# Kernel optimization log

Hardware: AMD Instinct MI355X
Metric: run time of the kernel (lower is better)

Reference implementation:

```python
import jax, jax.numpy as jnp
import numpy as np

LAM = 0.001  # init kwarg lam; agg='mean'


def setup_inputs() -> dict:
    key = jax.random.key(0)
    k1, k2 = jax.random.split(key)
    B, C, N = 4, 2, 8192
    inputs = jax.random.normal(k1, (B, C, N), dtype=jnp.float32)
    coords = jax.random.normal(k2, (B, N, 3), dtype=jnp.float32)
    return {"inputs": inputs, "coords": coords}


def _pairwise_dist(c):
    # c: (B, N, 3) -> (B, N, N) Euclidean distances (cdist p=2)
    sq = jnp.sum(c * c, axis=-1)                      # (B, N)
    d2 = sq[:, :, None] + sq[:, None, :] - 2.0 * jnp.einsum('bnd,bmd->bnm', c, c)
    return jnp.sqrt(jnp.maximum(d2, 0.0))


def reference(inputs, coords):
    coords = coords[:, :, :3]
    d = _pairwise_dist(coords)                        # (B, N, N)
    w = jax.nn.softmax(inputs, axis=1)[:, 1, :]       # (B, N) foreground prob
    dpp = d * w[:, :, None] * w[:, None, :]
    return jnp.mean(dpp) * LAM
```

## Files before the change

### kernel.cpp

```cpp
#include <hip/hip_runtime.h>

#define NFULL 8192
#define BATCH 4
#define NPTS (NFULL * BATCH)
#define TT 256
#define NT (NFULL / TT)
#define JOBS_PER_B (NT * (NT + 1) / 2)
#define TOTAL_JOBS (BATCH * JOBS_PER_B)
#define IR 4
#define IR2 (IR / 2)
#define JW 64
#define LAMBDA 0.001

typedef float f32x2 __attribute__((ext_vector_type(2)));

#define WS_PTS_OFF   0
#define WS_W_OFF     (NPTS * 16)
#define WS_PART_OFF  (WS_W_OFF + NPTS * 4)

__global__ __launch_bounds__(256)
void KUNi_prep(const float* __restrict__ inputs,
               const float* __restrict__ coords,
               float4* __restrict__ pts,
               float* __restrict__ wts) {
    const int idx = blockIdx.x * 256 + threadIdx.x;
    const int b = idx >> 13;
    const int n = idx & (NFULL - 1);
    const float* cp = coords + (size_t)idx * 3;
    const float x = cp[0], y = cp[1], z = cp[2];
    const float sq = fmaf(x, x, fmaf(y, y, z * z));
    const float a0 = inputs[(size_t)b * 2 * NFULL + n];
    const float a1 = inputs[(size_t)b * 2 * NFULL + NFULL + n];
    const float w = 1.0f / (1.0f + __expf(a0 - a1));
    pts[idx] = make_float4(x, y, z, sq);
    wts[idx] = w;
}

__global__ void KUNi_finalize(const float* __restrict__ partials,
                              float* __restrict__ out) {
    const int tid = threadIdx.x;
    const int lane = tid & 63, wv = tid >> 6;
    double s = 0.0;
    for (int i = tid; i < TOTAL_JOBS; i += 256) s += (double)partials[i];
#pragma unroll
    for (int off = 32; off > 0; off >>= 1) s += __shfl_xor(s, off, 64);
    __shared__ double sd[4];
    if (lane == 0) sd[wv] = s;
    __syncthreads();
    if (tid == 0) {
        const double scale = LAMBDA / ((double)BATCH * (double)NFULL * (double)NFULL);
        out[0] = (float)((sd[0] + sd[1] + sd[2] + sd[3]) * scale);
    }
}

__device__ __forceinline__ int tri_off(int t) {
    return t * (2 * NT + 1 - t) / 2;
}

__global__ __launch_bounds__(256)
void KUNi_dpp_kernel(const float4* __restrict__ pts,
                     const float* __restrict__ wts,
                     float* __restrict__ partials) {
    __shared__ float sred[4];

    const int tid = threadIdx.x;
    const int lane = tid & 63;
    const int wv = tid >> 6;
    const int bid = blockIdx.x;
    const int b = bid / JOBS_PER_B;
    const int p = bid - b * JOBS_PER_B;

    const float q = (float)(2 * NT + 1);
    int ti = (int)floorf((q - sqrtf(fmaf(-8.0f, (float)p, q * q))) * 0.5f);
    if (p < tri_off(ti)) --ti;
    else if (p >= tri_off(ti + 1)) ++ti;
    const int tj = ti + (p - tri_off(ti));
    const int base = b * NFULL;

    f32x2 ix2[IR2], iy2[IR2], iz2[IR2], isq2[IR2], iw2[IR2], acc2[IR2];
    const int ibase = base + ti * TT + lane;
#pragma unroll
    for (int k = 0; k < IR2; ++k) {
        const float4 p0 = pts[ibase + (2 * k) * 64];
        const float4 p1 = pts[ibase + (2 * k + 1) * 64];
        ix2[k]  = (f32x2){-2.0f * p0.x, -2.0f * p1.x};
        iy2[k]  = (f32x2){-2.0f * p0.y, -2.0f * p1.y};
        iz2[k]  = (f32x2){-2.0f * p0.z, -2.0f * p1.z};
        isq2[k] = (f32x2){p0.w, p1.w};
        iw2[k]  = (f32x2){wts[ibase + (2 * k) * 64],
                          wts[ibase + (2 * k + 1) * 64]};
        acc2[k] = (f32x2){0.0f, 0.0f};
    }

    const float4* __restrict__ pj = pts + base + tj * TT;
    const float* __restrict__ pw = wts + base + tj * TT;
    const int j0 = wv * JW;
#pragma unroll 4
    for (int jj = j0; jj < j0 + JW; ++jj) {
        const int ju = __builtin_amdgcn_readfirstlane(jj);
        const float4 jv = pj[ju];
        const float jw = pw[ju];
#pragma unroll
        for (int k = 0; k < IR2; ++k) {
            f32x2 t = isq2[k] + jv.w;
            t = __builtin_elementwise_fma(ix2[k], (f32x2){jv.x, jv.x}, t);
            t = __builtin_elementwise_fma(iy2[k], (f32x2){jv.y, jv.y}, t);
            t = __builtin_elementwise_fma(iz2[k], (f32x2){jv.z, jv.z}, t);
            t = __builtin_elementwise_max(t, (f32x2){0.0f, 0.0f});
            f32x2 s;
            s.x = __builtin_amdgcn_sqrtf(t.x);
            s.y = __builtin_amdgcn_sqrtf(t.y);
            acc2[k] = __builtin_elementwise_fma(s, (f32x2){jw, jw}, acc2[k]);
        }
    }

    f32x2 vv = iw2[0] * acc2[0];
#pragma unroll
    for (int k = 1; k < IR2; ++k)
        vv = __builtin_elementwise_fma(iw2[k], acc2[k], vv);
    float v = vv.x + vv.y;
    if (ti != tj) v *= 2.0f;

#pragma unroll
    for (int off = 32; off > 0; off >>= 1) v += __shfl_xor(v, off, 64);
    if (lane == 0) sred[wv] = v;
    __syncthreads();
    if (tid == 0) partials[bid] = sred[0] + sred[1] + sred[2] + sred[3];
}

extern "C" void kernel_launch(void* const* d_in, const int* in_sizes, int n_in,
                              void* d_out, int out_size, void* d_ws, size_t ws_size,
                              hipStream_t stream) {
    const float* inputs = (const float*)d_in[0];
    const float* coords = (const float*)d_in[1];
    float* out = (float*)d_out;
    char* ws = (char*)d_ws;
    float4* pts = (float4*)(ws + WS_PTS_OFF);
    float* wts = (float*)(ws + WS_W_OFF);
    float* partials = (float*)(ws + WS_PART_OFF);

    KUNi_prep<<<NPTS / 256, 256, 0, stream>>>(inputs, coords, pts, wts);
    KUNi_dpp_kernel<<<TOTAL_JOBS, 256, 0, stream>>>(pts, wts, partials);
    KUNi_finalize<<<1, 256, 0, stream>>>(partials, out);
}
```

Measured before the change: 92.10 us.

## Pair two i-tiles per block and stage j-tile in shared memory

Each block now processes two upper-triangular i-tiles against one j-tile, with 8 i-points per lane instead of 4. This halves the block count and doubles the reuse of each j-point load. The j-tile is pre-scaled and staged in LDS, then read as broadcasts, with weights fetched as float4 groups. The change is meant to cut per-block setup and global/scalar load overhead, at the cost of more registers, a loop to decode the tile pair, and some wasted work where the paired tile falls off the diagonal.

Result: faster. 87.95 us (-4.5%).

```diff
diff --git a/kernel.cpp b/kernel.cpp
--- a/kernel.cpp
+++ b/kernel.cpp
@@ -5,10 +5,9 @@
 #define NPTS (NFULL * BATCH)
 #define TT 256
 #define NT (NFULL / TT)
-#define JOBS_PER_B (NT * (NT + 1) / 2)
-#define TOTAL_JOBS (BATCH * JOBS_PER_B)
-#define IR 4
-#define IR2 (IR / 2)
+#define BLOCKS_PER_B 272
+#define TOTAL_BLOCKS (BATCH * BLOCKS_PER_B)
+#define IR2 4
 #define JW 64
 #define LAMBDA 0.001
 
@@ -41,7 +40,7 @@
     const int tid = threadIdx.x;
     const int lane = tid & 63, wv = tid >> 6;
     double s = 0.0;
-    for (int i = tid; i < TOTAL_JOBS; i += 256) s += (double)partials[i];
+    for (int i = tid; i < TOTAL_BLOCKS; i += 256) s += (double)partials[i];
 #pragma unroll
     for (int off = 32; off > 0; off >>= 1) s += __shfl_xor(s, off, 64);
     __shared__ double sd[4];
@@ -53,64 +52,74 @@
     }
 }
 
-__device__ __forceinline__ int tri_off(int t) {
-    return t * (2 * NT + 1 - t) / 2;
-}
-
 __global__ __launch_bounds__(256)
 void KUNi_dpp_kernel(const float4* __restrict__ pts,
                      const float* __restrict__ wts,
                      float* __restrict__ partials) {
+    __shared__ float4 sjA[TT];
+    __shared__ float sw[TT];
     __shared__ float sred[4];
 
     const int tid = threadIdx.x;
     const int lane = tid & 63;
     const int wv = tid >> 6;
     const int bid = blockIdx.x;
-    const int b = bid / JOBS_PER_B;
-    const int p = bid - b * JOBS_PER_B;
+    const int b = bid / BLOCKS_PER_B;
+    int r = bid - b * BLOCKS_PER_B;
 
-    const float q = (float)(2 * NT + 1);
-    int ti = (int)floorf((q - sqrtf(fmaf(-8.0f, (float)p, q * q))) * 0.5f);
-    if (p < tri_off(ti)) --ti;
-    else if (p >= tri_off(ti + 1)) ++ti;
-    const int tj = ti + (p - tri_off(ti));
+    int tj = 0;
+    while (r >= ((tj + 2) >> 1)) { r -= (tj + 2) >> 1; ++tj; }
+    const int ti0 = 2 * r;
+    const int t1v = 2 * r + 1;
+    const bool v1 = (t1v <= tj);
+    const int ti1 = v1 ? t1v : ti0;
+    const float fac0 = (ti0 != tj) ? 2.0f : 1.0f;
+    const float fac1 = v1 ? ((t1v != tj) ? 2.0f : 1.0f) : 0.0f;
     const int base = b * NFULL;
 
+    {
+        const float4 jp = pts[base + tj * TT + tid];
+        sjA[tid] = make_float4(-2.0f * jp.x, -2.0f * jp.y, -2.0f * jp.z, jp.w);
+        sw[tid] = wts[base + tj * TT + tid];
+    }
+
     f32x2 ix2[IR2], iy2[IR2], iz2[IR2], isq2[IR2], iw2[IR2], acc2[IR2];
-    const int ibase = base + ti * TT + lane;
+    const int ia = base + ti0 * TT + lane;
+    const int ib = base + ti1 * TT + lane;
 #pragma unroll
     for (int k = 0; k < IR2; ++k) {
-        const float4 p0 = pts[ibase + (2 * k) * 64];
-        const float4 p1 = pts[ibase + (2 * k + 1) * 64];
-        ix2[k]  = (f32x2){-2.0f * p0.x, -2.0f * p1.x};
-        iy2[k]  = (f32x2){-2.0f * p0.y, -2.0f * p1.y};
-        iz2[k]  = (f32x2){-2.0f * p0.z, -2.0f * p1.z};
+        const float4 p0 = pts[ia + k * 64];
+        const float4 p1 = pts[ib + k * 64];
+        ix2[k]  = (f32x2){p0.x, p1.x};
+        iy2[k]  = (f32x2){p0.y, p1.y};
+        iz2[k]  = (f32x2){p0.z, p1.z};
         isq2[k] = (f32x2){p0.w, p1.w};
-        iw2[k]  = (f32x2){wts[ibase + (2 * k) * 64],
-                          wts[ibase + (2 * k + 1) * 64]};
+        iw2[k]  = (f32x2){wts[ia + k * 64], wts[ib + k * 64]};
         acc2[k] = (f32x2){0.0f, 0.0f};
     }
 
-    const float4* __restrict__ pj = pts + base + tj * TT;
-    const float* __restrict__ pw = wts + base + tj * TT;
+    __syncthreads();
+
     const int j0 = wv * JW;
-#pragma unroll 4
-    for (int jj = j0; jj < j0 + JW; ++jj) {
-        const int ju = __builtin_amdgcn_readfirstlane(jj);
-        const float4 jv = pj[ju];
-        const float jw = pw[ju];
+#pragma unroll 2
+    for (int g = 0; g < JW / 4; ++g) {
+        const float4 w4 = *(const float4*)&sw[j0 + 4 * g];
 #pragma unroll
-        for (int k = 0; k < IR2; ++k) {
-            f32x2 t = isq2[k] + jv.w;
-            t = __builtin_elementwise_fma(ix2[k], (f32x2){jv.x, jv.x}, t);
-            t = __builtin_elementwise_fma(iy2[k], (f32x2){jv.y, jv.y}, t);
-            t = __builtin_elementwise_fma(iz2[k], (f32x2){jv.z, jv.z}, t);
-            t = __builtin_elementwise_max(t, (f32x2){0.0f, 0.0f});
-            f32x2 s;
-            s.x = __builtin_amdgcn_sqrtf(t.x);
-            s.y = __builtin_amdgcn_sqrtf(t.y);
-            acc2[k] = __builtin_elementwise_fma(s, (f32x2){jw, jw}, acc2[k]);
+        for (int u = 0; u < 4; ++u) {
+            const float4 jv = sjA[j0 + 4 * g + u];
+            const float jw = (&w4.x)[u];
+#pragma unroll
+            for (int k = 0; k < IR2; ++k) {
+                f32x2 t = isq2[k] + jv.w;
+                t = __builtin_elementwise_fma(ix2[k], (f32x2){jv.x, jv.x}, t);
+                t = __builtin_elementwise_fma(iy2[k], (f32x2){jv.y, jv.y}, t);
+                t = __builtin_elementwise_fma(iz2[k], (f32x2){jv.z, jv.z}, t);
+                t = __builtin_elementwise_max(t, (f32x2){0.0f, 0.0f});
+                f32x2 s;
+                s.x = __builtin_amdgcn_sqrtf(t.x);
+                s.y = __builtin_amdgcn_sqrtf(t.y);
+                acc2[k] = __builtin_elementwise_fma(s, (f32x2){jw, jw}, acc2[k]);
+            }
         }
     }
 
@@ -118,8 +127,7 @@
 #pragma unroll
     for (int k = 1; k < IR2; ++k)
         vv = __builtin_elementwise_fma(iw2[k], acc2[k], vv);
-    float v = vv.x + vv.y;
-    if (ti != tj) v *= 2.0f;
+    float v = fmaf(fac0, vv.x, fac1 * vv.y);
 
 #pragma unroll
     for (int off = 32; off > 0; off >>= 1) v += __shfl_xor(v, off, 64);
@@ -140,6 +148,6 @@
     float* partials = (float*)(ws + WS_PART_OFF);
 
     KUNi_prep<<<NPTS / 256, 256, 0, stream>>>(inputs, coords, pts, wts);
-    KUNi_dpp_kernel<<<TOTAL_JOBS, 256, 0, stream>>>(pts, wts, partials);
+    KUNi_dpp_kernel<<<TOTAL_BLOCKS, 256, 0, stream>>>(pts, wts, partials);
     KUNi_finalize<<<1, 256, 0, stream>>>(partials, out);
 }
```
